# Kernel tuning notes

Hardware: AMD Instinct MI355X
Metric: run time of the kernel (lower is better)

## Reference

```python
import jax, jax.numpy as jnp
import numpy as np

LEAKY_SLOPE = 0.01  # torch nn.LeakyReLU default

def _mlp(x, w1, b1, w2, b2):
    # MLP_Layer(num_layers=2, batch_norm=False): Linear -> ReLU -> Linear
    return jax.nn.relu(x @ w1 + b1) @ w2 + b2

def _edge_softmax(scores, dst, num_nodes):
    # softmax over incoming edges of each destination node; scores: [E, H]
    m = jax.ops.segment_max(scores, dst, num_segments=num_nodes)  # [N, H]
    e = jnp.exp(scores - m[dst])
    s = jax.ops.segment_sum(e, dst, num_segments=num_nodes)       # [N, H]
    return e / s[dst]

def setup_inputs() -> dict:
    key = jax.random.key(0)
    ks = jax.random.split(key, 10)
    N, E, H = 50000, 800000, 4
    D_H, PCA, PI, HID = 64, 64, 32, 128
    inp = {
        "h":    jax.random.normal(ks[0], (N, D_H), jnp.float32),
        "pca":  jax.random.normal(ks[1], (N, PCA), jnp.float32),
        "pimg": jax.random.normal(ks[2], (N, PI), jnp.float32),
        "pca_w1": jax.random.normal(ks[3], (2 * PCA, HID), jnp.float32) * (1.0 / np.sqrt(2 * PCA)),
        "pca_b1": jnp.zeros((HID,), jnp.float32),
        "pca_w2": jax.random.normal(ks[4], (HID, H), jnp.float32) * (1.0 / np.sqrt(HID)),
        "pca_b2": jnp.zeros((H,), jnp.float32),
        "pi_w1": jax.random.normal(ks[5], (2 * PI, HID), jnp.float32) * (1.0 / np.sqrt(2 * PI)),
        "pi_b1": jnp.zeros((HID,), jnp.float32),
        "pi_w2": jax.random.normal(ks[6], (HID, H), jnp.float32) * (1.0 / np.sqrt(HID)),
        "pi_b2": jnp.zeros((H,), jnp.float32),
        "src": jax.random.randint(ks[7], (E,), 0, N, jnp.int32),
        "dst": jax.random.randint(ks[8], (E,), 0, N, jnp.int32),
    }
    return inp

def reference(h, pca, pimg, pca_w1, pca_b1, pca_w2, pca_b2,
              pi_w1, pi_b1, pi_w2, pi_b2, src, dst):
    N = h.shape[0]

    def attend(feat, w1, b1, w2, b2):
        e_feat = jnp.concatenate([feat[src], feat[dst]], axis=1)        # [E, 2F]
        score = jax.nn.leaky_relu(_mlp(e_feat, w1, b1, w2, b2), LEAKY_SLOPE)  # [E, H]
        a = _edge_softmax(score, dst, N)                                # [E, H]
        msg = h[src][:, None, :] * a[:, :, None]                        # [E, H, D]
        return jax.ops.segment_sum(msg, dst, num_segments=N)           # [N, H, D]

    out_pca = attend(pca, pca_w1, pca_b1, pca_w2, pca_b2)
    out_pi = attend(pimg, pi_w1, pi_b1, pi_w2, pi_b2)
    return jnp.concatenate([out_pca, out_pi], axis=-1)                  # [N, H, 2D]
```

## Files before the change

### kernel.cpp

```cpp
#include <hip/hip_runtime.h>
#include <hip/hip_fp16.h>

constexpr int HID = 128;
constexpr int DH  = 64;

typedef _Float16 f16x2 __attribute__((ext_vector_type(2)));
struct F16x8 { f16x2 a, b, c, d; };

__device__ __forceinline__ float fdot2(f16x2 a, f16x2 b, float c) {
#if __has_builtin(__builtin_amdgcn_fdot2)
  return __builtin_amdgcn_fdot2(a, b, c, false);
#else
  return c + (float)a[0] * (float)b[0] + (float)a[1] * (float)b[1];
#endif
}

__device__ __forceinline__ f16x2 relu2(f16x2 x) {
  f16x2 z = {(_Float16)0, (_Float16)0};
#if __has_builtin(__builtin_elementwise_max)
  return __builtin_elementwise_max(x, z);
#else
  f16x2 r; r[0] = x[0] > z[0] ? x[0] : z[0]; r[1] = x[1] > z[1] ? x[1] : z[1]; return r;
#endif
}

template<int F, int NB>
__launch_bounds__(256)
__global__ void uv_kernel(const float* __restrict__ feat, const float* __restrict__ w1,
                          const float* __restrict__ b1,
                          _Float16* __restrict__ u_cat, _Float16* __restrict__ v_cat,
                          int roff, int N) {
  __shared__ float sfeat[NB][F + 1];
  int nb = blockIdx.x * NB;
  for (int i = threadIdx.x; i < NB * F; i += 256) {
    int n = i / F, k = i - n * F;
    int gn = nb + n;
    sfeat[n][k] = (gn < N) ? feat[(size_t)gn * F + k] : 0.f;
  }
  __syncthreads();
  int j = threadIdx.x & 127;
  int g = threadIdx.x >> 7;
  constexpr int NPT = NB / 2;
  float ua[NPT], va[NPT];
#pragma unroll
  for (int i = 0; i < NPT; i++) { ua[i] = 0.f; va[i] = 0.f; }
  for (int k = 0; k < F; k++) {
    float wu = w1[k * HID + j];
    float wv = w1[(F + k) * HID + j];
#pragma unroll
    for (int i = 0; i < NPT; i++) {
      float f = sfeat[g * NPT + i][k];
      ua[i] = fmaf(f, wu, ua[i]);
      va[i] = fmaf(f, wv, va[i]);
    }
  }
  float b1v = b1[j];
#pragma unroll
  for (int i = 0; i < NPT; i++) {
    int gn = nb + g * NPT + i;
    if (gn < N) {
      u_cat[(size_t)gn * 256 + roff + j] = (_Float16)ua[i];
      v_cat[(size_t)gn * 256 + roff + j] = (_Float16)(va[i] + b1v);
    }
  }
}

__global__ void h16_kernel(const float* __restrict__ h, _Float16* __restrict__ h16, int total) {
  int i = (blockIdx.x * 256 + threadIdx.x) * 4;
  if (i + 3 < total) {
    float4 v = *(const float4*)(h + i);
    h16[i] = (_Float16)v.x; h16[i + 1] = (_Float16)v.y;
    h16[i + 2] = (_Float16)v.z; h16[i + 3] = (_Float16)v.w;
  } else {
    for (int q = 0; q < 4; q++) if (i + q < total) h16[i + q] = (_Float16)h[i + q];
  }
}

__global__ void count_kernel(const int* __restrict__ dst, int* __restrict__ counts, int E) {
  int e = blockIdx.x * 256 + threadIdx.x;
  if (e < E) atomicAdd(&counts[dst[e]], 1);
}

__launch_bounds__(256)
__global__ void scan1_kernel(const int* __restrict__ counts, int* __restrict__ bsums, int N) {
  int b = blockIdx.x, tid = threadIdx.x;
  int base = b * 1024 + tid * 4;
  int s = 0;
  if (base + 3 < N) {
    int4 v = *(const int4*)(counts + base);
    s = v.x + v.y + v.z + v.w;
  } else {
    for (int q = 0; q < 4; q++) { int idx = base + q; if (idx < N) s += counts[idx]; }
  }
#pragma unroll
  for (int o = 32; o >= 1; o >>= 1) s += __shfl_xor(s, o);
  __shared__ int ws[4];
  if ((tid & 63) == 0) ws[tid >> 6] = s;
  __syncthreads();
  if (tid == 0) bsums[b] = ws[0] + ws[1] + ws[2] + ws[3];
}

__launch_bounds__(1024)
__global__ void scan2_kernel(const int* __restrict__ bsums, int* __restrict__ bpre,
                             int* __restrict__ offsets, int NB, int N, int E) {
  int tid = threadIdx.x, lane = tid & 63, w = tid >> 6;
  int v = (tid < NB) ? bsums[tid] : 0;
  int incl = v;
#pragma unroll
  for (int o = 1; o < 64; o <<= 1) { int t = __shfl_up(incl, o); if (lane >= o) incl += t; }
  __shared__ int ws[16];
  if (lane == 63) ws[w] = incl;
  __syncthreads();
  int wpre = 0;
  for (int q = 0; q < w; q++) wpre += ws[q];
  if (tid < NB) bpre[tid] = wpre + incl - v;
  if (tid == 0) offsets[N] = E;
}

__launch_bounds__(256)
__global__ void scan3_kernel(const int* __restrict__ counts, const int* __restrict__ bpre,
                             int* __restrict__ offsets, int N) {
  int b = blockIdx.x, tid = threadIdx.x, lane = tid & 63, w = tid >> 6;
  int base = b * 1024 + tid * 4;
  int c[4] = {0, 0, 0, 0};
  if (base + 3 < N) {
    int4 v = *(const int4*)(counts + base);
    c[0] = v.x; c[1] = v.y; c[2] = v.z; c[3] = v.w;
  } else {
    for (int q = 0; q < 4; q++) { int idx = base + q; if (idx < N) c[q] = counts[idx]; }
  }
  int s = c[0] + c[1] + c[2] + c[3];
  int incl = s;
#pragma unroll
  for (int o = 1; o < 64; o <<= 1) { int t = __shfl_up(incl, o); if (lane >= o) incl += t; }
  int excl = incl - s;
  __shared__ int ws[4];
  if (lane == 63) ws[w] = incl;
  __syncthreads();
  int wpre = 0;
  for (int q = 0; q < w; q++) wpre += ws[q];
  int off = bpre[b] + wpre + excl;
  for (int q = 0; q < 4; q++) {
    int idx = base + q;
    if (idx < N) offsets[idx] = off;
    off += c[q];
  }
}

__global__ void fill_kernel(const int* __restrict__ src, const int* __restrict__ dst,
                            const int* __restrict__ offsets, int* __restrict__ cursor,
                            int* __restrict__ src_sorted, int* __restrict__ dst_sorted, int E) {
  int e = blockIdx.x * 256 + threadIdx.x;
  if (e < E) {
    int d = dst[e];
    int pos = offsets[d] + atomicAdd(&cursor[d], 1);
    src_sorted[pos] = src[e];
    dst_sorted[pos] = d;
  }
}

__launch_bounds__(256, 4)
__global__ void score_kernel(const _Float16* __restrict__ u_cat, const _Float16* __restrict__ v_cat,
                             const int* __restrict__ src_sorted, const int* __restrict__ dst_sorted,
                             const float* __restrict__ w2a, const float* __restrict__ w2b,
                             const float* __restrict__ b2a, const float* __restrict__ b2b,
                             float* __restrict__ ek, int E) {
  __shared__ _Float16 s_w2[1024];
  int tid = threadIdx.x;
  for (int i = tid; i < 1024; i += 256) {
    int c = i >> 5, k = (i >> 3) & 3, jj = i & 7;
    int rel = c >> 4, j = (c & 15) * 8 + jj;
    float val = rel ? w2b[j * 4 + k] : w2a[j * 4 + k];
    s_w2[i] = (_Float16)val;
  }
  __syncthreads();
  int e = blockIdx.x * 256 + tid;
  if (e >= E) return;
  int s = src_sorted[e], d = dst_sorted[e];

  float acc[8];
#pragma unroll
  for (int k = 0; k < 4; k++) { acc[k] = b2a[k]; acc[4 + k] = b2b[k]; }

  const F16x8* up = (const F16x8*)(u_cat + (size_t)s * 256);
  const F16x8* vp = (const F16x8*)(v_cat + (size_t)d * 256);
#pragma unroll 4
  for (int c = 0; c < 32; c++) {
    int ko = (c >> 4) << 2;
    F16x8 ua = up[c], va = vp[c];
    f16x2 h0 = relu2(ua.a + va.a), h1 = relu2(ua.b + va.b);
    f16x2 h2 = relu2(ua.c + va.c), h3 = relu2(ua.d + va.d);
    const f16x2* wp = (const f16x2*)(s_w2 + c * 32);
#pragma unroll
    for (int k = 0; k < 4; k++) {
      f16x2 w0 = wp[k * 4 + 0], w1 = wp[k * 4 + 1], w2v = wp[k * 4 + 2], w3 = wp[k * 4 + 3];
      float t = acc[ko + k];
      t = fdot2(h0, w0, t); t = fdot2(h1, w1, t);
      t = fdot2(h2, w2v, t); t = fdot2(h3, w3, t);
      acc[ko + k] = t;
    }
  }
  float r[8];
#pragma unroll
  for (int k = 0; k < 8; k++) {
    float x = acc[k]; x = x > 0.f ? x : 0.01f * x; r[k] = __expf(x);
  }
  float* ep = ek + (size_t)e * 8;
  *(float4*)(ep + 0) = make_float4(r[0], r[1], r[2], r[3]);
  *(float4*)(ep + 4) = make_float4(r[4], r[5], r[6], r[7]);
}

__launch_bounds__(256)
__global__ void agg_kernel(const float* __restrict__ ek, const int* __restrict__ src_sorted,
                           const int* __restrict__ offsets, const _Float16* __restrict__ h16,
                           float* __restrict__ out, int N) {
  int wid = blockIdx.x * 4 + (threadIdx.x >> 6);
  int lane = threadIdx.x & 63;
  if (wid >= N) return;
  int off0 = offsets[wid], off1 = offsets[wid + 1];
  int deg = off1 - off0;
  float* op = out + (size_t)wid * 512;
  if (deg == 0) {
#pragma unroll
    for (int k = 0; k < 4; k++) { op[k * 128 + lane] = 0.f; op[k * 128 + 64 + lane] = 0.f; }
    return;
  }
  float accO[8] = {0, 0, 0, 0, 0, 0, 0, 0};
  float ssum[8] = {0, 0, 0, 0, 0, 0, 0, 0};
  int jj = 0;
  for (; jj + 2 <= deg; jj += 2) {
    size_t e0 = (size_t)(off0 + jj);
    const float4* p0 = (const float4*)(ek + e0 * 8);
    float4 a0 = p0[0], a1 = p0[1], b0 = p0[2], b1 = p0[3];
    int sa = src_sorted[e0], sb = src_sorted[e0 + 1];
    float hva = (float)h16[(size_t)sa * DH + lane];
    float hvb = (float)h16[(size_t)sb * DH + lane];
    accO[0] = fmaf(a0.x, hva, accO[0]); accO[1] = fmaf(a0.y, hva, accO[1]);
    accO[2] = fmaf(a0.z, hva, accO[2]); accO[3] = fmaf(a0.w, hva, accO[3]);
    accO[4] = fmaf(a1.x, hva, accO[4]); accO[5] = fmaf(a1.y, hva, accO[5]);
    accO[6] = fmaf(a1.z, hva, accO[6]); accO[7] = fmaf(a1.w, hva, accO[7]);
    accO[0] = fmaf(b0.x, hvb, accO[0]); accO[1] = fmaf(b0.y, hvb, accO[1]);
    accO[2] = fmaf(b0.z, hvb, accO[2]); accO[3] = fmaf(b0.w, hvb, accO[3]);
    accO[4] = fmaf(b1.x, hvb, accO[4]); accO[5] = fmaf(b1.y, hvb, accO[5]);
    accO[6] = fmaf(b1.z, hvb, accO[6]); accO[7] = fmaf(b1.w, hvb, accO[7]);
    ssum[0] += a0.x + b0.x; ssum[1] += a0.y + b0.y;
    ssum[2] += a0.z + b0.z; ssum[3] += a0.w + b0.w;
    ssum[4] += a1.x + b1.x; ssum[5] += a1.y + b1.y;
    ssum[6] += a1.z + b1.z; ssum[7] += a1.w + b1.w;
  }
  if (jj < deg) {
    size_t e0 = (size_t)(off0 + jj);
    const float4* p0 = (const float4*)(ek + e0 * 8);
    float4 a0 = p0[0], a1 = p0[1];
    int sa = src_sorted[e0];
    float hva = (float)h16[(size_t)sa * DH + lane];
    accO[0] = fmaf(a0.x, hva, accO[0]); accO[1] = fmaf(a0.y, hva, accO[1]);
    accO[2] = fmaf(a0.z, hva, accO[2]); accO[3] = fmaf(a0.w, hva, accO[3]);
    accO[4] = fmaf(a1.x, hva, accO[4]); accO[5] = fmaf(a1.y, hva, accO[5]);
    accO[6] = fmaf(a1.z, hva, accO[6]); accO[7] = fmaf(a1.w, hva, accO[7]);
    ssum[0] += a0.x; ssum[1] += a0.y; ssum[2] += a0.z; ssum[3] += a0.w;
    ssum[4] += a1.x; ssum[5] += a1.y; ssum[6] += a1.z; ssum[7] += a1.w;
  }
#pragma unroll
  for (int k = 0; k < 8; k++) {
    float rsv = 1.f / ssum[k];
    int col = k < 4 ? k * 128 + lane : (k - 4) * 128 + 64 + lane;
    op[col] = accO[k] * rsv;
  }
}

extern "C" void kernel_launch(void* const* d_in, const int* in_sizes, int n_in,
                              void* d_out, int out_size, void* d_ws, size_t ws_size,
                              hipStream_t stream) {
  const float* h      = (const float*)d_in[0];
  const float* pca    = (const float*)d_in[1];
  const float* pimg   = (const float*)d_in[2];
  const float* pca_w1 = (const float*)d_in[3];
  const float* pca_b1 = (const float*)d_in[4];
  const float* pca_w2 = (const float*)d_in[5];
  const float* pca_b2 = (const float*)d_in[6];
  const float* pi_w1  = (const float*)d_in[7];
  const float* pi_b1  = (const float*)d_in[8];
  const float* pi_w2  = (const float*)d_in[9];
  const float* pi_b2  = (const float*)d_in[10];
  const int*   src    = (const int*)d_in[11];
  const int*   dst    = (const int*)d_in[12];
  int N = in_sizes[0] / 64;
  int E = in_sizes[11];
  float* out = (float*)d_out;

  char* ws = (char*)d_ws;
  size_t o = 0;
  auto alloc = [&](size_t bytes) { void* p = ws + o; o += (bytes + 255) & ~(size_t)255; return p; };
  _Float16* u_cat = (_Float16*)alloc((size_t)N * 256 * 2);
  _Float16* v_cat = (_Float16*)alloc((size_t)N * 256 * 2);
  _Float16* h16   = (_Float16*)alloc((size_t)N * 64 * 2);
  int* counts  = (int*)alloc((size_t)N * 4);
  int* cursor  = (int*)alloc((size_t)N * 4);
  int* offsets = (int*)alloc((size_t)(N + 1) * 4);
  int* bsums   = (int*)alloc(1024 * 4);
  int* bpre    = (int*)alloc(1024 * 4);
  int* src_sorted = (int*)alloc((size_t)E * 4);
  int* dst_sorted = (int*)alloc((size_t)E * 4);
  float* ek       = (float*)alloc((size_t)E * 8 * 4);

  hipMemsetAsync(counts, 0, (size_t)N * 4, stream);
  hipMemsetAsync(cursor, 0, (size_t)N * 4, stream);

  uv_kernel<64, 32><<<(N + 31) / 32, 256, 0, stream>>>(pca, pca_w1, pca_b1, u_cat, v_cat, 0, N);
  uv_kernel<32, 32><<<(N + 31) / 32, 256, 0, stream>>>(pimg, pi_w1, pi_b1, u_cat, v_cat, 128, N);
  h16_kernel<<<((N * 64) / 4 + 255) / 256, 256, 0, stream>>>(h, h16, N * 64);
  count_kernel<<<(E + 255) / 256, 256, 0, stream>>>(dst, counts, E);
  int NB = (N + 1023) / 1024;
  scan1_kernel<<<NB, 256, 0, stream>>>(counts, bsums, N);
  scan2_kernel<<<1, 1024, 0, stream>>>(bsums, bpre, offsets, NB, N, E);
  scan3_kernel<<<NB, 256, 0, stream>>>(counts, bpre, offsets, N);
  fill_kernel<<<(E + 255) / 256, 256, 0, stream>>>(src, dst, offsets, cursor, src_sorted, dst_sorted, E);
  score_kernel<<<(E + 255) / 256, 256, 0, stream>>>(u_cat, v_cat, src_sorted, dst_sorted,
                                                    pca_w2, pi_w2, pca_b2, pi_b2, ek, E);
  agg_kernel<<<(N + 3) / 4, 256, 0, stream>>>(ek, src_sorted, offsets, h16, out, N);
}
```

Measured before the change: 330.1 us.

## Compute edge score second layer with MFMA 16x16x32 f16 instead of fdot2

Replaces the per-thread fdot2 loop in the score kernel with wave-level MFMA. Each wave stages 64 edges' relu hidden vectors in LDS, then multiplies them against a register-resident W2 fragment (both relations packed into 8 of 16 columns). The goal is to offload the second MLP layer's arithmetic to matrix cores. In exchange it adds LDS traffic, wastes half the MFMA columns, and writes ek with scattered scalar stores. The kernel is likely gather-bound on u/v rows, so the gain may be limited.

```diff
diff --git a/kernel.cpp b/kernel.cpp
--- a/kernel.cpp
+++ b/kernel.cpp
@@ -5,22 +5,18 @@
 constexpr int DH  = 64;
 
 typedef _Float16 f16x2 __attribute__((ext_vector_type(2)));
-struct F16x8 { f16x2 a, b, c, d; };
-
-__device__ __forceinline__ float fdot2(f16x2 a, f16x2 b, float c) {
-#if __has_builtin(__builtin_amdgcn_fdot2)
-  return __builtin_amdgcn_fdot2(a, b, c, false);
-#else
-  return c + (float)a[0] * (float)b[0] + (float)a[1] * (float)b[1];
-#endif
-}
-
-__device__ __forceinline__ f16x2 relu2(f16x2 x) {
-  f16x2 z = {(_Float16)0, (_Float16)0};
+typedef _Float16 fh8   __attribute__((ext_vector_type(8)));
+typedef float    f32x4v __attribute__((ext_vector_type(4)));
+
+__device__ __forceinline__ fh8 relu8(fh8 x) {
+  fh8 z = {0, 0, 0, 0, 0, 0, 0, 0};
 #if __has_builtin(__builtin_elementwise_max)
   return __builtin_elementwise_max(x, z);
 #else
-  f16x2 r; r[0] = x[0] > z[0] ? x[0] : z[0]; r[1] = x[1] > z[1] ? x[1] : z[1]; return r;
+  fh8 r;
+#pragma unroll
+  for (int i = 0; i < 8; i++) r[i] = x[i] > z[i] ? x[i] : z[i];
+  return r;
 #endif
 }
 
@@ -165,49 +161,72 @@
                              const float* __restrict__ w2a, const float* __restrict__ w2b,
                              const float* __restrict__ b2a, const float* __restrict__ b2b,
                              float* __restrict__ ek, int E) {
-  __shared__ _Float16 s_w2[1024];
-  int tid = threadIdx.x;
-  for (int i = tid; i < 1024; i += 256) {
-    int c = i >> 5, k = (i >> 3) & 3, jj = i & 7;
-    int rel = c >> 4, j = (c & 15) * 8 + jj;
-    float val = rel ? w2b[j * 4 + k] : w2a[j * 4 + k];
-    s_w2[i] = (_Float16)val;
-  }
-  __syncthreads();
-  int e = blockIdx.x * 256 + tid;
-  if (e >= E) return;
-  int s = src_sorted[e], d = dst_sorted[e];
-
-  float acc[8];
-#pragma unroll
-  for (int k = 0; k < 4; k++) { acc[k] = b2a[k]; acc[4 + k] = b2b[k]; }
-
-  const F16x8* up = (const F16x8*)(u_cat + (size_t)s * 256);
-  const F16x8* vp = (const F16x8*)(v_cat + (size_t)d * 256);
-#pragma unroll 4
-  for (int c = 0; c < 32; c++) {
-    int ko = (c >> 4) << 2;
-    F16x8 ua = up[c], va = vp[c];
-    f16x2 h0 = relu2(ua.a + va.a), h1 = relu2(ua.b + va.b);
-    f16x2 h2 = relu2(ua.c + va.c), h3 = relu2(ua.d + va.d);
-    const f16x2* wp = (const f16x2*)(s_w2 + c * 32);
-#pragma unroll
-    for (int k = 0; k < 4; k++) {
-      f16x2 w0 = wp[k * 4 + 0], w1 = wp[k * 4 + 1], w2v = wp[k * 4 + 2], w3 = wp[k * 4 + 3];
-      float t = acc[ko + k];
-      t = fdot2(h0, w0, t); t = fdot2(h1, w1, t);
-      t = fdot2(h2, w2v, t); t = fdot2(h3, w3, t);
-      acc[ko + k] = t;
-    }
-  }
-  float r[8];
-#pragma unroll
-  for (int k = 0; k < 8; k++) {
-    float x = acc[k]; x = x > 0.f ? x : 0.01f * x; r[k] = __expf(x);
-  }
-  float* ep = ek + (size_t)e * 8;
-  *(float4*)(ep + 0) = make_float4(r[0], r[1], r[2], r[3]);
-  *(float4*)(ep + 4) = make_float4(r[4], r[5], r[6], r[7]);
+  __shared__ _Float16 sA[4 * 64 * 40];
+  int tid = threadIdx.x, lane = tid & 63, w = tid >> 6;
+  int col = lane & 15, kg = lane >> 4;
+  int ebase = blockIdx.x * 256 + w * 64;
+  int e = ebase + lane;
+  bool valid = e < E;
+  int s = valid ? src_sorted[e] : 0;
+  int d = valid ? dst_sorted[e] : 0;
+
+  fh8 bfrag[8];
+#pragma unroll
+  for (int t = 0; t < 8; t++) {
+#pragma unroll
+    for (int j = 0; j < 8; j++) {
+      int k = t * 32 + kg * 8 + j;
+      float wv = 0.f;
+      if (col < 4) { if (k < 128) wv = w2a[k * 4 + col]; }
+      else if (col < 8) { if (k >= 128) wv = w2b[(k - 128) * 4 + (col - 4)]; }
+      bfrag[t][j] = (_Float16)wv;
+    }
+  }
+
+  f32x4v acc[4];
+#pragma unroll
+  for (int m = 0; m < 4; m++) acc[m] = (f32x4v){0.f, 0.f, 0.f, 0.f};
+
+  _Float16* myA = sA + w * (64 * 40);
+  const fh8* up = (const fh8*)(u_cat + (size_t)s * 256);
+  const fh8* vp = (const fh8*)(v_cat + (size_t)d * 256);
+
+#pragma unroll 2
+  for (int t = 0; t < 8; t++) {
+    fh8 h0 = relu8(up[t * 4 + 0] + vp[t * 4 + 0]);
+    fh8 h1 = relu8(up[t * 4 + 1] + vp[t * 4 + 1]);
+    fh8 h2 = relu8(up[t * 4 + 2] + vp[t * 4 + 2]);
+    fh8 h3 = relu8(up[t * 4 + 3] + vp[t * 4 + 3]);
+    _Float16* rp = myA + lane * 40;
+    *(fh8*)(rp + 0)  = h0;
+    *(fh8*)(rp + 8)  = h1;
+    *(fh8*)(rp + 16) = h2;
+    *(fh8*)(rp + 24) = h3;
+    __builtin_amdgcn_wave_barrier();
+    asm volatile("s_waitcnt lgkmcnt(0)" ::: "memory");
+#pragma unroll
+    for (int m = 0; m < 4; m++) {
+      fh8 af = *(const fh8*)(myA + (m * 16 + col) * 40 + kg * 8);
+      acc[m] = __builtin_amdgcn_mfma_f32_16x16x32_f16(af, bfrag[t], acc[m], 0, 0, 0);
+    }
+    __builtin_amdgcn_wave_barrier();
+  }
+
+  if (col < 8) {
+    float b2v = (col < 4) ? b2a[col] : b2b[col - 4];
+#pragma unroll
+    for (int m = 0; m < 4; m++) {
+#pragma unroll
+      for (int q = 0; q < 4; q++) {
+        int er = ebase + m * 16 + kg * 4 + q;
+        if (er < E) {
+          float x = acc[m][q] + b2v;
+          x = x > 0.f ? x : 0.01f * x;
+          ek[(size_t)er * 8 + col] = __expf(x);
+        }
+      }
+    }
+  }
 }
 
 __launch_bounds__(256)
```

Result: slower. 480.8 us (+45.7%).
